# Kernel optimization log

Hardware: AMD Instinct MI355X
Metric: run time of the kernel (lower is better)

Reference implementation:

```python
import jax, jax.numpy as jnp
import numpy as np

B, S, D_IN, D_FC1, NB = 16384, 256, 2048, 1024, 10

def setup_inputs() -> dict:
    key = jax.random.key(0)
    k1, k2, k3, k4 = jax.random.split(key, 4)
    return {
        "input_feats": jax.random.normal(k1, (B, D_IN), dtype=jnp.float32),
        "w1": jax.random.normal(k2, (D_IN, D_FC1), dtype=jnp.float32) * 0.02,
        "b1": jnp.zeros((D_FC1,), dtype=jnp.float32),
        "w_shape": jax.random.normal(k3, (D_FC1, 2 * NB), dtype=jnp.float32) * 0.02,
        "b_shape": jnp.zeros((2 * NB,), dtype=jnp.float32),
        "noise": jax.random.normal(k4, (B, S, NB), dtype=jnp.float32),
        "num_samples": S,
    }

def reference(input_feats, w1, b1, w_shape, b_shape, noise, num_samples):
    # x = ELU(fc1(input_feats))
    x = jax.nn.elu(input_feats @ w1 + b1)                      # (B, 1024)
    shape_params = x @ w_shape + b_shape                       # (B, 20)
    shape_mode = shape_params[:, :NB]                          # (B, 10)
    shape_log_std = shape_params[:, NB:]                       # (B, 10)
    # Normal(mode, exp(log_std)).rsample([num_samples]).transpose(0,1)
    # reparameterized with externalized eps -> (B, num_samples, 10)
    shape_samples = shape_mode[:, None, :] + jnp.exp(shape_log_std)[:, None, :] * noise
    return shape_mode, shape_log_std, shape_samples
```

## Files before the change

### kernel.cpp

```cpp
#include <hip/hip_runtime.h>
#include <stdint.h>

using f32x4  = __attribute__((ext_vector_type(4))) float;
using bf16x8 = __attribute__((ext_vector_type(8))) short;
using ushort8 = __attribute__((ext_vector_type(8))) unsigned short;

#define B_   16384
#define S_   256
#define DIN  2048
#define DFC  1024
#define NB_  10

__device__ __forceinline__ unsigned short f2bf(float f) {
  union { float f; unsigned int u; } v; v.f = f;
  unsigned int u = v.u;
  unsigned int r = (u + 0x7FFFu + ((u >> 16) & 1u)) >> 16;
  return (unsigned short)r;
}

__device__ __forceinline__ void gload_lds16(const void* g, void* l) {
  __builtin_amdgcn_global_load_lds(
      (const __attribute__((address_space(1))) unsigned int*)g,
      (__attribute__((address_space(3))) unsigned int*)l, 16, 0, 0);
}

__global__ __launch_bounds__(256)
void convT_kernel(const float* __restrict__ W, unsigned short* __restrict__ Wt) {
  __shared__ unsigned short t[32][33];
  const int tx = threadIdx.x & 31;
  const int ty = threadIdx.x >> 5;
  const int nb = blockIdx.x * 32;
  const int kb = blockIdx.y * 32;
#pragma unroll
  for (int i = 0; i < 32; i += 8)
    t[ty + i][tx] = f2bf(W[(size_t)(kb + ty + i) * DFC + nb + tx]);
  __syncthreads();
#pragma unroll
  for (int i = 0; i < 32; i += 8)
    Wt[(size_t)(nb + ty + i) * DIN + kb + tx] = t[tx][ty + i];
}

__global__ __launch_bounds__(256)
void convA_kernel(const float* __restrict__ A, unsigned short* __restrict__ Ab) {
  const size_t total = (size_t)B_ * DIN;
  size_t idx = ((size_t)blockIdx.x * 256 + threadIdx.x) * 8;
  const size_t stride = (size_t)gridDim.x * 256 * 8;
  for (; idx < total; idx += stride) {
    f32x4 a = *(const f32x4*)(A + idx);
    f32x4 b = *(const f32x4*)(A + idx + 4);
    ushort8 o;
    o[0] = f2bf(a[0]); o[1] = f2bf(a[1]); o[2] = f2bf(a[2]); o[3] = f2bf(a[3]);
    o[4] = f2bf(b[0]); o[5] = f2bf(b[1]); o[6] = f2bf(b[2]); o[7] = f2bf(b[3]);
    *(ushort8*)(Ab + idx) = o;
  }
}

__global__ __launch_bounds__(512, 2)
void gemm1_kernel(const unsigned short* __restrict__ Ab, const unsigned short* __restrict__ Bt,
                  const float* __restrict__ b1, unsigned short* __restrict__ X) {
  __shared__ unsigned short sT[2][2][2][8192];
  const int tid  = threadIdx.x;
  const int wave = tid >> 6, lane = tid & 63;
  const int wm = wave >> 2, wn = wave & 3;
  const int b = blockIdx.x;
  const int tile = (b & 7) * 32 + (b >> 3);
  const int mtile = tile >> 2, ntile = tile & 3;
  const int rowBase = mtile * 256, colBase = ntile * 256;

  f32x4 acc[8][4] = {};

  const int lrow0 = wave * 16 + (lane >> 3);
  const int q     = (lane & 7) ^ (lrow0 & 7);
  const unsigned short* gA = Ab + (size_t)(rowBase + lrow0 * 2 + (q >> 2)) * DIN + (q & 3) * 8;
  const unsigned short* gB = Bt + (size_t)(colBase + lrow0 * 2 + (q >> 2)) * DIN + (q & 3) * 8;
  const int ldOff = wave * 1024;

  const int frow = lane & 15, hi = lane >> 4, fr2 = frow >> 1;
  const int pp    = ((frow & 1) * 4 + hi) ^ (fr2 & 7);
  const int aBase = (wm * 64 + fr2) * 64 + pp * 8;
  const int bBase = (wn * 32 + fr2) * 64 + pp * 8;

#define STAGE(opv, db, ksv, kt) do {                                        \
    const unsigned short* g_ = ((opv) ? gB : gA) + (kt) * 64 + (ksv) * 32;  \
    unsigned short* l_ = &sT[db][opv][ksv][ldOff];                          \
    gload_lds16(g_, l_);                                                    \
    gload_lds16(g_ + (size_t)16 * DIN, l_ + 512);                           \
  } while (0)

  bf16x8 afr[4], bfr[4];
#define READ_B(db, ksv) do {                                                \
    const unsigned short* s_ = &sT[db][1][ksv][bBase];                      \
    bfr[0] = *(const bf16x8*)(s_);        bfr[1] = *(const bf16x8*)(s_ + 512); \
    bfr[2] = *(const bf16x8*)(s_ + 1024); bfr[3] = *(const bf16x8*)(s_ + 1536); \
  } while (0)
#define READ_A(db, ksv, mq) do {                                            \
    const unsigned short* s_ = &sT[db][0][ksv][aBase + (mq) * 2048];        \
    afr[0] = *(const bf16x8*)(s_);        afr[1] = *(const bf16x8*)(s_ + 512); \
    afr[2] = *(const bf16x8*)(s_ + 1024); afr[3] = *(const bf16x8*)(s_ + 1536); \
  } while (0)
#define MFMA16(mq) do {                                                     \
    __builtin_amdgcn_s_setprio(1);                                          \
    _Pragma("unroll") for (int m_ = 0; m_ < 4; ++m_)                        \
      _Pragma("unroll") for (int n_ = 0; n_ < 4; ++n_)                      \
        acc[(mq) * 4 + m_][n_] = __builtin_amdgcn_mfma_f32_16x16x32_bf16(   \
            afr[m_], bfr[n_], acc[(mq) * 4 + m_][n_], 0, 0, 0);             \
    __builtin_amdgcn_s_setprio(0);                                          \
  } while (0)
#define FENCE asm volatile("" ::: "memory")
#define BAR do { FENCE; __builtin_amdgcn_s_barrier(); FENCE; } while (0)

  STAGE(0, 0, 0, 0); STAGE(1, 0, 0, 0); STAGE(0, 0, 1, 0); STAGE(1, 0, 1, 0);
  STAGE(0, 1, 0, 1); STAGE(1, 1, 0, 1);

  const int NT = DIN / 64;
#pragma unroll 2
  for (int k = 0; k < NT - 1; ++k) {
    const int db = k & 1, dn = db ^ 1;
    asm volatile("s_waitcnt vmcnt(8)" ::: "memory");
    BAR;
    READ_B(db, 0); READ_A(db, 0, 0);
    STAGE(0, dn, 1, k + 1);
    MFMA16(0);
    BAR;
    READ_A(db, 0, 1);
    STAGE(1, dn, 1, k + 1);
    MFMA16(1);
    asm volatile("s_waitcnt vmcnt(8)" ::: "memory");
    BAR;
    READ_B(db, 1); READ_A(db, 1, 0);
    if (k < NT - 2) STAGE(0, db, 0, k + 2);
    MFMA16(0);
    BAR;
    READ_A(db, 1, 1);
    if (k < NT - 2) STAGE(1, db, 0, k + 2);
    MFMA16(1);
  }
  {
    const int db = (NT - 1) & 1;
    asm volatile("s_waitcnt vmcnt(4)" ::: "memory");
    BAR;
    READ_B(db, 0); READ_A(db, 0, 0);
    MFMA16(0);
    BAR;
    READ_A(db, 0, 1);
    MFMA16(1);
    asm volatile("s_waitcnt vmcnt(0)" ::: "memory");
    BAR;
    READ_B(db, 1); READ_A(db, 1, 0);
    MFMA16(0);
    BAR;
    READ_A(db, 1, 1);
    MFMA16(1);
  }
#undef STAGE
#undef READ_A
#undef READ_B
#undef MFMA16

  const int er0 = rowBase + wm * 128 + hi * 4;
  const int ec0 = colBase + wn * 64 + frow;
  float bv[4];
#pragma unroll
  for (int n = 0; n < 4; ++n) bv[n] = b1[ec0 + n * 16];
#pragma unroll
  for (int m = 0; m < 8; ++m)
#pragma unroll
    for (int n = 0; n < 4; ++n)
#pragma unroll
      for (int r = 0; r < 4; ++r) {
        float v = acc[m][n][r] + bv[n];
        v = v > 0.f ? v : expm1f(v);
        X[(size_t)(er0 + m * 16 + r) * DFC + ec0 + n * 16] = f2bf(v);
      }
}

__global__ __launch_bounds__(256)
void gemm2_kernel(const unsigned short* __restrict__ X, const float* __restrict__ Wsh,
                  const float* __restrict__ bsh, float* __restrict__ out) {
  __shared__ unsigned short sX[64 * 32];
  __shared__ unsigned short sW[32 * 40];
  const int tid  = threadIdx.x;
  const int wave = tid >> 6, lane = tid & 63;
  const int rowB = blockIdx.x * 64;
  f32x4 acc[2] = {};
  const unsigned short* xp = X + (size_t)(rowB + (tid >> 2)) * DFC + (tid & 3) * 8;
  unsigned short* sXb = &sX[wave * 512];
  const int frow = lane & 15, fks = (lane >> 4) * 8;

  for (int kk = 0; kk < DFC; kk += 32) {
    gload_lds16(xp + kk, sXb);
    for (int idx = tid; idx < 32 * 40; idx += 256) {
      int j = idx / 40, ki = idx - j * 40;
      sW[idx] = (j < 20 && ki < 32) ? f2bf(Wsh[(size_t)(kk + ki) * 20 + j]) : (unsigned short)0;
    }
    __syncthreads();
    bf16x8 xa  = *(const bf16x8*)&sX[(wave * 16 + frow) * 32 + fks];
    bf16x8 w0  = *(const bf16x8*)&sW[(frow) * 40 + fks];
    bf16x8 w1f = *(const bf16x8*)&sW[(16 + frow) * 40 + fks];
    acc[0] = __builtin_amdgcn_mfma_f32_16x16x32_bf16(xa, w0,  acc[0], 0, 0, 0);
    acc[1] = __builtin_amdgcn_mfma_f32_16x16x32_bf16(xa, w1f, acc[1], 0, 0, 0);
    __syncthreads();
  }
  const int r0 = rowB + wave * 16 + (lane >> 4) * 4;
  const int c0 = lane & 15;
#pragma unroll
  for (int n = 0; n < 2; ++n) {
    int j = n * 16 + c0;
    if (j < 20) {
      float bj = bsh[j];
      int jj = j < 10 ? j : j - 10;
      size_t base = (j < 10) ? (size_t)0 : (size_t)B_ * NB_;
#pragma unroll
      for (int r = 0; r < 4; ++r)
        out[base + (size_t)(r0 + r) * NB_ + jj] = acc[n][r] + bj;
    }
  }
}

__global__ __launch_bounds__(256)
void sample_kernel(const float* __restrict__ noise, float* __restrict__ out) {
  __shared__ float sm[4][NB_], se[4][NB_];
  const int tid  = threadIdx.x;
  const int wave = tid >> 6, lane = tid & 63;
  const int row  = blockIdx.x * 4 + wave;
  if (lane < NB_) {
    sm[wave][lane] = out[(size_t)row * NB_ + lane];
    se[wave][lane] = expf(out[(size_t)B_ * NB_ + (size_t)row * NB_ + lane]);
  }
  __syncthreads();
  const f32x4* np4 = (const f32x4*)(noise + (size_t)row * (S_ * NB_));
  f32x4*       op4 = (f32x4*)(out + (size_t)2 * B_ * NB_ + (size_t)row * (S_ * NB_));
#pragma unroll
  for (int it = 0; it < (S_ * NB_) / 256; ++it) {
    f32x4 nv = np4[it * 64 + lane];
    int j0 = (lane * 4 + it * 6) % 10;
    int j1 = j0 + 1; if (j1 >= 10) j1 -= 10;
    int j2 = j1 + 1; if (j2 >= 10) j2 -= 10;
    int j3 = j2 + 1; if (j3 >= 10) j3 -= 10;
    f32x4 r;
    r[0] = sm[wave][j0] + se[wave][j0] * nv[0];
    r[1] = sm[wave][j1] + se[wave][j1] * nv[1];
    r[2] = sm[wave][j2] + se[wave][j2] * nv[2];
    r[3] = sm[wave][j3] + se[wave][j3] * nv[3];
    op4[it * 64 + lane] = r;
  }
}

extern "C" void kernel_launch(void* const* d_in, const int* in_sizes, int n_in,
                              void* d_out, int out_size, void* d_ws, size_t ws_size,
                              hipStream_t stream) {
  const float* A     = (const float*)d_in[0];
  const float* W1    = (const float*)d_in[1];
  const float* b1    = (const float*)d_in[2];
  const float* Wsh   = (const float*)d_in[3];
  const float* bsh   = (const float*)d_in[4];
  const float* noise = (const float*)d_in[5];
  float* out = (float*)d_out;

  unsigned short* Wt = (unsigned short*)d_ws;
  unsigned short* X  = (unsigned short*)d_ws + (size_t)DFC * DIN;
  const size_t wsNeed = (size_t)DFC * DIN * 2 + (size_t)B_ * DFC * 2 + (size_t)B_ * DIN * 2;
  unsigned short* Ab = (ws_size >= wsNeed)
      ? (unsigned short*)d_ws + (size_t)DFC * DIN + (size_t)B_ * DFC
      : (unsigned short*)(out + (size_t)2 * B_ * NB_);

  convT_kernel<<<dim3(DFC / 32, DIN / 32), 256, 0, stream>>>(W1, Wt);
  convA_kernel<<<dim3(2048), 256, 0, stream>>>(A, Ab);
  gemm1_kernel<<<dim3((B_ / 256) * (DFC / 256)), 512, 0, stream>>>(Ab, Wt, b1, X);
  gemm2_kernel<<<dim3(B_ / 64), 256, 0, stream>>>(X, Wsh, bsh, out);
  sample_kernel<<<dim3(B_ / 4), 256, 0, stream>>>(noise, out);
}
```

Before: 217.1 us.

## Restructure gemm2 with pre-transposed bf16 weights, full-row LDS staging and split-K

Adds a small kernel that converts and transposes the shape weights to bf16 once, so gemm2 no longer re-converts fp32 weights into LDS on every 32-wide K step. gemm2 now loads a full 32x1024 bf16 row block into swizzled LDS in one pass, reads the weights directly from global memory, and splits K across wave pairs with an LDS reduction. This removes the per-iteration barriers and the repeated conversion work. The cost is an extra launch and a much larger LDS footprint per block, which may lower occupancy. The gemm1 swizzle expression is also simplified (fr2 is under 8, so behaviour is unchanged).

```diff
diff --git a/kernel.cpp b/kernel.cpp
--- a/kernel.cpp
+++ b/kernel.cpp
@@ -38,6 +38,13 @@
 #pragma unroll
   for (int i = 0; i < 32; i += 8)
     Wt[(size_t)(nb + ty + i) * DIN + kb + tx] = t[tx][ty + i];
+}
+
+__global__ __launch_bounds__(256)
+void convW2_kernel(const float* __restrict__ Wsh, unsigned short* __restrict__ WshT) {
+  const int idx = blockIdx.x * 256 + threadIdx.x;
+  const int j = idx >> 10, k = idx & 1023;
+  WshT[idx] = (j < 20) ? f2bf(Wsh[(size_t)k * 20 + j]) : (unsigned short)0;
 }
 
 __global__ __launch_bounds__(256)
@@ -76,7 +83,7 @@
   const int ldOff = wave * 1024;
 
   const int frow = lane & 15, hi = lane >> 4, fr2 = frow >> 1;
-  const int pp    = ((frow & 1) * 4 + hi) ^ (fr2 & 7);
+  const int pp    = ((frow & 1) * 4 + hi) ^ fr2;
   const int aBase = (wm * 64 + fr2) * 64 + pp * 8;
   const int bBase = (wn * 32 + fr2) * 64 + pp * 8;
 
@@ -175,44 +182,65 @@
 }
 
 __global__ __launch_bounds__(256)
-void gemm2_kernel(const unsigned short* __restrict__ X, const float* __restrict__ Wsh,
+void gemm2_kernel(const unsigned short* __restrict__ X, const unsigned short* __restrict__ WshT,
                   const float* __restrict__ bsh, float* __restrict__ out) {
-  __shared__ unsigned short sX[64 * 32];
-  __shared__ unsigned short sW[32 * 40];
-  const int tid  = threadIdx.x;
-  const int wave = tid >> 6, lane = tid & 63;
-  const int rowB = blockIdx.x * 64;
+  __shared__ unsigned short sX[32 * 1024];
+  __shared__ float sRed[32][22];
+  const int tid = threadIdx.x, wave = tid >> 6, lane = tid & 63;
+  const int rh = wave & 1, kh = wave >> 1;
+  const int rowB = blockIdx.x * 32;
+  const int frow = lane & 15, hi = lane >> 4;
+
+#pragma unroll
+  for (int i = 0; i < 16; ++i) {
+    const int ji = wave * 16 + i;
+    const int r  = ji >> 1;
+    const int ph = (ji & 1) * 64 + lane;
+    const int c  = ph ^ (r & 7);
+    gload_lds16(X + (size_t)(rowB + r) * DFC + c * 8, &sX[ji * 512]);
+  }
+  asm volatile("s_waitcnt vmcnt(0)" ::: "memory");
+  __syncthreads();
+
   f32x4 acc[2] = {};
-  const unsigned short* xp = X + (size_t)(rowB + (tid >> 2)) * DFC + (tid & 3) * 8;
-  unsigned short* sXb = &sX[wave * 512];
-  const int frow = lane & 15, fks = (lane >> 4) * 8;
-
-  for (int kk = 0; kk < DFC; kk += 32) {
-    gload_lds16(xp + kk, sXb);
-    for (int idx = tid; idx < 32 * 40; idx += 256) {
-      int j = idx / 40, ki = idx - j * 40;
-      sW[idx] = (j < 20 && ki < 32) ? f2bf(Wsh[(size_t)(kk + ki) * 20 + j]) : (unsigned short)0;
+  const int arow = rh * 16 + frow;
+  const unsigned short* bp0 = WshT + (size_t)frow * DFC + kh * 512 + hi * 8;
+  const unsigned short* bp1 = WshT + (size_t)(16 + frow) * DFC + kh * 512 + hi * 8;
+#pragma unroll
+  for (int s = 0; s < 16; ++s) {
+    const int c = kh * 64 + s * 4 + hi;
+    const int p = c ^ (arow & 7);
+    bf16x8 xa = *(const bf16x8*)&sX[arow * 1024 + p * 8];
+    bf16x8 b0 = *(const bf16x8*)(bp0 + s * 32);
+    bf16x8 b1 = *(const bf16x8*)(bp1 + s * 32);
+    acc[0] = __builtin_amdgcn_mfma_f32_16x16x32_bf16(xa, b0, acc[0], 0, 0, 0);
+    acc[1] = __builtin_amdgcn_mfma_f32_16x16x32_bf16(xa, b1, acc[1], 0, 0, 0);
+  }
+
+  const int r0l = rh * 16 + hi * 4;
+  if (kh == 1) {
+#pragma unroll
+    for (int n = 0; n < 2; ++n) {
+      const int j = n * 16 + frow;
+      if (j < 20)
+#pragma unroll
+        for (int r = 0; r < 4; ++r)
+          sRed[r0l + r][j] = acc[n][r];
     }
-    __syncthreads();
-    bf16x8 xa  = *(const bf16x8*)&sX[(wave * 16 + frow) * 32 + fks];
-    bf16x8 w0  = *(const bf16x8*)&sW[(frow) * 40 + fks];
-    bf16x8 w1f = *(const bf16x8*)&sW[(16 + frow) * 40 + fks];
-    acc[0] = __builtin_amdgcn_mfma_f32_16x16x32_bf16(xa, w0,  acc[0], 0, 0, 0);
-    acc[1] = __builtin_amdgcn_mfma_f32_16x16x32_bf16(xa, w1f, acc[1], 0, 0, 0);
-    __syncthreads();
-  }
-  const int r0 = rowB + wave * 16 + (lane >> 4) * 4;
-  const int c0 = lane & 15;
-#pragma unroll
-  for (int n = 0; n < 2; ++n) {
-    int j = n * 16 + c0;
-    if (j < 20) {
-      float bj = bsh[j];
-      int jj = j < 10 ? j : j - 10;
-      size_t base = (j < 10) ? (size_t)0 : (size_t)B_ * NB_;
-#pragma unroll
-      for (int r = 0; r < 4; ++r)
-        out[base + (size_t)(r0 + r) * NB_ + jj] = acc[n][r] + bj;
+  }
+  __syncthreads();
+  if (kh == 0) {
+#pragma unroll
+    for (int n = 0; n < 2; ++n) {
+      const int j = n * 16 + frow;
+      if (j < 20) {
+        const float bj = bsh[j];
+        const int jj = j < 10 ? j : j - 10;
+        const size_t base = (j < 10) ? (size_t)0 : (size_t)B_ * NB_;
+#pragma unroll
+        for (int r = 0; r < 4; ++r)
+          out[base + (size_t)(rowB + r0l + r) * NB_ + jj] = acc[n][r] + sRed[r0l + r][j] + bj;
+      }
     }
   }
 }
@@ -257,16 +285,18 @@
   const float* noise = (const float*)d_in[5];
   float* out = (float*)d_out;
 
-  unsigned short* Wt = (unsigned short*)d_ws;
-  unsigned short* X  = (unsigned short*)d_ws + (size_t)DFC * DIN;
-  const size_t wsNeed = (size_t)DFC * DIN * 2 + (size_t)B_ * DFC * 2 + (size_t)B_ * DIN * 2;
+  unsigned short* Wt   = (unsigned short*)d_ws;
+  unsigned short* X    = Wt + (size_t)DFC * DIN;
+  unsigned short* WshT = X + (size_t)B_ * DFC;
+  const size_t wsNeed = ((size_t)DFC * DIN + (size_t)B_ * DFC + 32 * 1024 + (size_t)B_ * DIN) * 2;
   unsigned short* Ab = (ws_size >= wsNeed)
-      ? (unsigned short*)d_ws + (size_t)DFC * DIN + (size_t)B_ * DFC
+      ? WshT + (size_t)32 * 1024
       : (unsigned short*)(out + (size_t)2 * B_ * NB_);
 
   convT_kernel<<<dim3(DFC / 32, DIN / 32), 256, 0, stream>>>(W1, Wt);
+  convW2_kernel<<<dim3(128), 256, 0, stream>>>(Wsh, WshT);
   convA_kernel<<<dim3(2048), 256, 0, stream>>>(A, Ab);
   gemm1_kernel<<<dim3((B_ / 256) * (DFC / 256)), 512, 0, stream>>>(Ab, Wt, b1, X);
-  gemm2_kernel<<<dim3(B_ / 64), 256, 0, stream>>>(X, Wsh, bsh, out);
+  gemm2_kernel<<<dim3(B_ / 32), 256, 0, stream>>>(X, WshT, bsh, out);
   sample_kernel<<<dim3(B_ / 4), 256, 0, stream>>>(noise, out);
 }
```

After: 229.9 us. 1.06x slower.
